# Kernel tuning notes

Hardware: AMD Instinct MI355X
Metric: run time of the kernel (lower is better)

## Reference

```python
import jax, jax.numpy as jnp
import numpy as np

L, D, H, T, B = 4, 512, 8, 1024, 8
FF = 4 * D          # 2048
E = 2
EC = E * D          # 1024 conv channels
K = 31
W = 64              # attention window
DH = D // H
EPS = 1e-5


def _ln(x, g, b):
    m = jnp.mean(x, axis=-1, keepdims=True)
    v = jnp.mean((x - m) ** 2, axis=-1, keepdims=True)
    return (x - m) * jax.lax.rsqrt(v + EPS) * g + b


def setup_inputs() -> dict:
    key = jax.random.key(0)
    ks = iter(jax.random.split(key, 64))
    n = lambda shape, s=0.02: jax.random.normal(next(ks), shape, dtype=jnp.float32) * s
    inp = {
        'x': jax.random.normal(next(ks), (B, T, D), dtype=jnp.float32),
        # FFN1 (half residual)
        'ffn1_ln_g': jnp.ones((L, D)), 'ffn1_ln_b': jnp.zeros((L, D)),
        'ffn1_w1': n((L, D, FF)), 'ffn1_b1': jnp.zeros((L, FF)),
        'ffn1_w2': n((L, FF, D)), 'ffn1_b2': jnp.zeros((L, D)),
        # local MHSA
        'attn_ln_g': jnp.ones((L, D)), 'attn_ln_b': jnp.zeros((L, D)),
        'qkv_w': n((L, D, 3 * D)), 'qkv_b': jnp.zeros((L, 3 * D)),
        'outp_w': n((L, D, D)), 'outp_b': jnp.zeros((L, D)),
        # conv module
        'conv_ln_g': jnp.ones((L, D)), 'conv_ln_b': jnp.zeros((L, D)),
        'pw1_w': n((L, D, 2 * EC)), 'pw1_b': jnp.zeros((L, 2 * EC)),
        'dw_w': n((L, EC, 1, K), 0.1), 'dw_b': jnp.zeros((L, EC)),
        'gn_g': jnp.ones((L, EC)), 'gn_b': jnp.zeros((L, EC)),
        'pw2_w': n((L, EC, D)), 'pw2_b': jnp.zeros((L, D)),
        # FFN2 (half residual)
        'ffn2_ln_g': jnp.ones((L, D)), 'ffn2_ln_b': jnp.zeros((L, D)),
        'ffn2_w1': n((L, D, FF)), 'ffn2_b1': jnp.zeros((L, FF)),
        'ffn2_w2': n((L, FF, D)), 'ffn2_b2': jnp.zeros((L, D)),
        # per-block final LN and decoder final LN
        'blk_ln_g': jnp.ones((L, D)), 'blk_ln_b': jnp.zeros((L, D)),
        'final_ln_g': jnp.ones((D,)), 'final_ln_b': jnp.zeros((D,)),
    }
    return inp


def _forward(x, ffn1_ln_g, ffn1_ln_b, ffn1_w1, ffn1_b1, ffn1_w2, ffn1_b2,
             attn_ln_g, attn_ln_b, qkv_w, qkv_b, outp_w, outp_b,
             conv_ln_g, conv_ln_b, pw1_w, pw1_b, dw_w, dw_b, gn_g, gn_b, pw2_w, pw2_b,
             ffn2_ln_g, ffn2_ln_b, ffn2_w1, ffn2_b1, ffn2_w2, ffn2_b2,
             blk_ln_g, blk_ln_b, final_ln_g, final_ln_b):
    t = jnp.arange(T)
    local_ok = jnp.abs(t[:, None] - t[None, :]) <= (W // 2)   # [T,T] banded window mask
    scale = DH ** -0.5

    for l in range(L):
        # ---- FFN1 (half residual), SiLU ----
        h = _ln(x, ffn1_ln_g[l], ffn1_ln_b[l])
        h = jax.nn.silu(h @ ffn1_w1[l] + ffn1_b1[l]) @ ffn1_w2[l] + ffn1_b2[l]
        x = x + 0.5 * h

        # ---- local windowed MHSA ----
        a = _ln(x, attn_ln_g[l], attn_ln_b[l])
        qkv = (a @ qkv_w[l] + qkv_b[l]).reshape(B, T, 3, H, DH)
        q, k, v = (qkv[:, :, 0].transpose(0, 2, 1, 3),  # [B,H,T,DH]
                   qkv[:, :, 1].transpose(0, 2, 1, 3),
                   qkv[:, :, 2].transpose(0, 2, 1, 3))
        scores = jnp.einsum('bhqd,bhkd->bhqk', q, k) * scale
        scores = jnp.where(local_ok, scores, -jnp.inf)
        attn = jax.nn.softmax(scores, axis=-1)
        o = jnp.einsum('bhqk,bhkd->bhqd', attn, v)
        o = o.transpose(0, 2, 1, 3).reshape(B, T, D)
        x = x + (o @ outp_w[l] + outp_b[l])

        # ---- convolution module ----
        c = _ln(x, conv_ln_g[l], conv_ln_b[l])
        c = c @ pw1_w[l] + pw1_b[l]                 # [B,T,2EC]
        c = c[..., :EC] * jax.nn.sigmoid(c[..., EC:])  # GLU (channel halves)
        c = c.transpose(0, 2, 1)                    # [B,EC,T]
        c = jax.lax.conv_general_dilated(
            c, dw_w[l], window_strides=(1,), padding=[((K - 1) // 2, (K - 1) // 2)],
            dimension_numbers=('NCH', 'OIH', 'NCH'), feature_group_count=EC)
        c = c + dw_b[l][None, :, None]
        # GroupNorm(num_groups=1): normalize over (C,T) per sample
        m = jnp.mean(c, axis=(1, 2), keepdims=True)
        vv = jnp.mean((c - m) ** 2, axis=(1, 2), keepdims=True)
        c = (c - m) * jax.lax.rsqrt(vv + EPS) * gn_g[l][None, :, None] + gn_b[l][None, :, None]
        c = jax.nn.silu(c)
        c = c.transpose(0, 2, 1) @ pw2_w[l] + pw2_b[l]  # [B,T,D]
        x = x + c

        # ---- FFN2 (half residual) ----
        h = _ln(x, ffn2_ln_g[l], ffn2_ln_b[l])
        h = jax.nn.silu(h @ ffn2_w1[l] + ffn2_b1[l]) @ ffn2_w2[l] + ffn2_b2[l]
        x = x + 0.5 * h

        # ---- per-block final LayerNorm ----
        x = _ln(x, blk_ln_g[l], blk_ln_b[l])

    return _ln(x, final_ln_g, final_ln_b)


def reference(x, ffn1_ln_g, ffn1_ln_b, ffn1_w1, ffn1_b1, ffn1_w2, ffn1_b2,
              attn_ln_g, attn_ln_b, qkv_w, qkv_b, outp_w, outp_b,
              conv_ln_g, conv_ln_b, pw1_w, pw1_b, dw_w, dw_b, gn_g, gn_b, pw2_w, pw2_b,
              ffn2_ln_g, ffn2_ln_b, ffn2_w1, ffn2_b1, ffn2_w2, ffn2_b2,
              blk_ln_g, blk_ln_b, final_ln_g, final_ln_b):
    return _forward(x, ffn1_ln_g, ffn1_ln_b, ffn1_w1, ffn1_b1, ffn1_w2, ffn1_b2,
                    attn_ln_g, attn_ln_b, qkv_w, qkv_b, outp_w, outp_b,
                    conv_ln_g, conv_ln_b, pw1_w, pw1_b, dw_w, dw_b, gn_g, gn_b, pw2_w, pw2_b,
                    ffn2_ln_g, ffn2_ln_b, ffn2_w1, ffn2_b1, ffn2_w2, ffn2_b2,
                    blk_ln_g, blk_ln_b, final_ln_g, final_ln_b)
```

## Files before the change

kernel.cpp:

```cpp
#include <hip/hip_runtime.h>
#include <hip/hip_bf16.h>
#include <math.h>

#define L_ 4
#define D_ 512
#define H_ 8
#define T_ 1024
#define B_ 8
#define FF_ 2048
#define EC_ 1024
#define KW_ 31
#define DH_ 64
#define ROWS (B_*T_)

typedef __attribute__((ext_vector_type(8))) short short8;
typedef __attribute__((ext_vector_type(4))) float f32x4;
typedef __attribute__((ext_vector_type(4))) unsigned short ushort4v;
typedef __attribute__((ext_vector_type(2))) unsigned short ushort2v;

static __device__ __forceinline__ unsigned short f2bf(float f) {
  __hip_bfloat16 h = __float2bfloat16(f);
  unsigned short u;
  __builtin_memcpy(&u, &h, 2);
  return u;
}
static __device__ __forceinline__ float bf2f(unsigned short h) {
  union { unsigned u; float f; } v; v.u = ((unsigned)h) << 16;
  return v.f;
}
static __device__ __forceinline__ float sigm(float x) {
  return __builtin_amdgcn_rcpf(1.0f + __expf(-x));
}

#define GLDS(gp, lp) __builtin_amdgcn_global_load_lds( \
    (const __attribute__((address_space(1))) unsigned int*)(const void*)(gp), \
    (__attribute__((address_space(3))) unsigned int*)(void*)(lp), 16, 0, 0)

#define SW8(row, slot) ((slot) ^ (((row) ^ ((row) >> 3)) & 7))

__global__ __launch_bounds__(256) void cvt_kernel(const float* __restrict__ in,
                                                  unsigned short* __restrict__ out)
{
  size_t i = ((size_t)blockIdx.x * 256 + threadIdx.x) * 8;
  float4 v0 = *(const float4*)(in + i);
  float4 v1 = *(const float4*)(in + i + 4);
  float vv[8] = {v0.x, v0.y, v0.z, v0.w, v1.x, v1.y, v1.z, v1.w};
  short8 o;
#pragma unroll
  for (int j = 0; j < 8; ++j) o[j] = (short)f2bf(vv[j]);
  *(short8*)(out + i) = o;
}

__global__ __launch_bounds__(256) void ln_bf16_kernel(const unsigned short* __restrict__ x,
    const float* __restrict__ g, const float* __restrict__ b, unsigned short* __restrict__ y)
{
  int row = blockIdx.x * 4 + (threadIdx.x >> 6);
  int l = threadIdx.x & 63;
  short8 xr = *(const short8*)(x + (size_t)row * D_ + l * 8);
  float vv[8];
#pragma unroll
  for (int j = 0; j < 8; ++j) vv[j] = bf2f((unsigned short)xr[j]);
  float s = 0.f, s2 = 0.f;
#pragma unroll
  for (int j = 0; j < 8; ++j) { s += vv[j]; s2 += vv[j] * vv[j]; }
#pragma unroll
  for (int off = 32; off; off >>= 1) {
    s  += __shfl_xor(s,  off, 64);
    s2 += __shfl_xor(s2, off, 64);
  }
  float mean = s * (1.0f / D_);
  float var  = s2 * (1.0f / D_) - mean * mean;
  float r = __builtin_amdgcn_rsqf(var + 1e-5f);
  float4 g0 = *(const float4*)(g + l * 8);
  float4 g1 = *(const float4*)(g + l * 8 + 4);
  float4 b0 = *(const float4*)(b + l * 8);
  float4 b1 = *(const float4*)(b + l * 8 + 4);
  float gg[8] = {g0.x, g0.y, g0.z, g0.w, g1.x, g1.y, g1.z, g1.w};
  float bb[8] = {b0.x, b0.y, b0.z, b0.w, b1.x, b1.y, b1.z, b1.w};
  short8 o;
#pragma unroll
  for (int j = 0; j < 8; ++j) o[j] = (short)f2bf((vv[j] - mean) * r * gg[j] + bb[j]);
  *(short8*)(y + (size_t)row * D_ + l * 8) = o;
}

template<bool BF2>
__global__ __launch_bounds__(256) void ln_dual_kernel(const unsigned short* __restrict__ x,
    const float* __restrict__ g1, const float* __restrict__ b1,
    const float* __restrict__ g2, const float* __restrict__ b2,
    unsigned short* __restrict__ y1, void* __restrict__ y2)
{
  int row = blockIdx.x * 4 + (threadIdx.x >> 6);
  int l = threadIdx.x & 63;
  short8 xr = *(const short8*)(x + (size_t)row * D_ + l * 8);
  float vv[8];
#pragma unroll
  for (int j = 0; j < 8; ++j) vv[j] = bf2f((unsigned short)xr[j]);
  float s = 0.f, s2 = 0.f;
#pragma unroll
  for (int j = 0; j < 8; ++j) { s += vv[j]; s2 += vv[j] * vv[j]; }
#pragma unroll
  for (int off = 32; off; off >>= 1) {
    s  += __shfl_xor(s,  off, 64);
    s2 += __shfl_xor(s2, off, 64);
  }
  float mean = s * (1.0f / D_);
  float var  = s2 * (1.0f / D_) - mean * mean;
  float r = __builtin_amdgcn_rsqf(var + 1e-5f);
  float4 g0 = *(const float4*)(g1 + l * 8);
  float4 g1v = *(const float4*)(g1 + l * 8 + 4);
  float4 b0 = *(const float4*)(b1 + l * 8);
  float4 b1v = *(const float4*)(b1 + l * 8 + 4);
  float ga[8] = {g0.x, g0.y, g0.z, g0.w, g1v.x, g1v.y, g1v.z, g1v.w};
  float ba[8] = {b0.x, b0.y, b0.z, b0.w, b1v.x, b1v.y, b1v.z, b1v.w};
  float yv[8];
  float u = 0.f, u2 = 0.f;
#pragma unroll
  for (int j = 0; j < 8; ++j) {
    yv[j] = (vv[j] - mean) * r * ga[j] + ba[j];
    u += yv[j]; u2 += yv[j] * yv[j];
  }
  {
    short8 o;
#pragma unroll
    for (int j = 0; j < 8; ++j) o[j] = (short)f2bf(yv[j]);
    *(short8*)(y1 + (size_t)row * D_ + l * 8) = o;
  }
#pragma unroll
  for (int off = 32; off; off >>= 1) {
    u  += __shfl_xor(u,  off, 64);
    u2 += __shfl_xor(u2, off, 64);
  }
  float mean2 = u * (1.0f / D_);
  float var2  = u2 * (1.0f / D_) - mean2 * mean2;
  float r2 = __builtin_amdgcn_rsqf(var2 + 1e-5f);
  float4 c0 = *(const float4*)(g2 + l * 8);
  float4 c1 = *(const float4*)(g2 + l * 8 + 4);
  float4 d0 = *(const float4*)(b2 + l * 8);
  float4 d1 = *(const float4*)(b2 + l * 8 + 4);
  float gc[8] = {c0.x, c0.y, c0.z, c0.w, c1.x, c1.y, c1.z, c1.w};
  float bc[8] = {d0.x, d0.y, d0.z, d0.w, d1.x, d1.y, d1.z, d1.w};
  if constexpr (BF2) {
    short8 o;
#pragma unroll
    for (int j = 0; j < 8; ++j) o[j] = (short)f2bf((yv[j] - mean2) * r2 * gc[j] + bc[j]);
    *(short8*)((unsigned short*)y2 + (size_t)row * D_ + l * 8) = o;
  } else {
    float z[8];
#pragma unroll
    for (int j = 0; j < 8; ++j) z[j] = (yv[j] - mean2) * r2 * gc[j] + bc[j];
    float4 o0 = {z[0], z[1], z[2], z[3]};
    float4 o1 = {z[4], z[5], z[6], z[7]};
    float* yp = (float*)y2 + (size_t)row * D_ + l * 8;
    *(float4*)yp = o0; *(float4*)(yp + 4) = o1;
  }
}

__global__ __launch_bounds__(256) void wtr_kernel(const float* __restrict__ W,
    unsigned short* __restrict__ Wt, int K, int N)
{
  __shared__ float tile[32][33];
  const float* Wl = W + (size_t)blockIdx.z * K * N;
  unsigned short* Wtl = Wt + (size_t)blockIdx.z * K * N;
  int n0 = blockIdx.x * 32, k0 = blockIdx.y * 32;
  int c = threadIdx.x & 31, r = threadIdx.x >> 5;
#pragma unroll
  for (int it = 0; it < 4; ++it) {
    int kk = r + it * 8;
    tile[kk][c] = Wl[(size_t)(k0 + kk) * N + n0 + c];
  }
  __syncthreads();
#pragma unroll
  for (int it = 0; it < 4; ++it) {
    int nn = r + it * 8;
    Wtl[(size_t)(n0 + nn) * K + k0 + c] = f2bf(tile[c][nn]);
  }
}

template<int EPI>
__global__ __launch_bounds__(256) void gemm_mfma(
    const unsigned short* __restrict__ A, const unsigned short* __restrict__ Wt,
    const float* __restrict__ bias, void* __restrict__ Cv,
    int N, int K)
{
  constexpr int TM = 128;
  constexpr int AI = TM / 32;
  __shared__ __align__(16) unsigned short As[3][TM * 32];
  __shared__ __align__(16) unsigned short Bs[3][128 * 32];
  int t = threadIdx.x;
  int gx = gridDim.x;
  int nwg = gx * gridDim.y;
  int orig = blockIdx.y * gx + blockIdx.x;
  int lg = (orig & 7) * (nwg >> 3) + (orig >> 3);
  int row0 = (lg / gx) * TM;
  int col0 = (lg % gx) * (EPI == 3 ? 64 : 128);
  int l = t & 63, w = t >> 6, wm = w >> 1, wn = w & 1;

  int ar0 = t >> 2;
  int sa0 = (t & 3) ^ ((ar0 >> 1) & 3);
  int ar1 = (t + 256) >> 2;
  int sa1 = (t & 3) ^ ((ar1 >> 1) & 3);
  const unsigned short* agp0 = A + (size_t)(row0 + ar0) * K + sa0 * 8;
  const unsigned short* agp1 = A + (size_t)(row0 + ar1) * K + sa1 * 8;
  const unsigned short* bgp0 = Wt + (size_t)(col0 + ar0) * K + sa0 * 8;
  const unsigned short* bgp1 =
      (EPI == 3) ? Wt + (size_t)(EC_ + col0 + (ar1 - 64)) * K + sa1 * 8
                 : Wt + (size_t)(col0 + ar1) * K + sa1 * 8;

  int lrow = (l >> 4) * 4, lcol = l & 15, kq = l >> 4;
  int aoff[AI], boff[4];
#pragma unroll
  for (int i = 0; i < AI; ++i) {
    int row = wm * (TM / 2) + i * 16 + lcol;
    aoff[i] = (row * 4 + (kq ^ ((row >> 1) & 3))) * 8;
  }
#pragma unroll
  for (int j = 0; j < 4; ++j) {
    int row;
    if constexpr (EPI == 3)
      row = (j < 2 ? wn * 32 + j * 16 : 64 + wn * 32 + (j - 2) * 16) + lcol;
    else
      row = wn * 64 + j * 16 + lcol;
    boff[j] = (row * 4 + (kq ^ ((row >> 1) & 3))) * 8;
  }

  f32x4 acc[AI][4] = {};
  int nt = K >> 5;

  auto stage = [&](int buf) {
    GLDS(agp0, As[buf] + t * 8);
    GLDS(agp1, As[buf] + (t + 256) * 8);
    GLDS(bgp0, Bs[buf] + t * 8);
    GLDS(bgp1, Bs[buf] + (t + 256) * 8);
    agp0 += 32; agp1 += 32; bgp0 += 32; bgp1 += 32;
  };
  stage(0); stage(1);
  int cur = 0, nxt = 2;

  for (int kt = 0; kt < nt; ++kt) {
    if (kt < nt - 1) asm volatile("s_waitcnt vmcnt(4)" ::: "memory");
    else             asm volatile("s_waitcnt vmcnt(0)" ::: "memory");
    __builtin_amdgcn_s_barrier();
    __builtin_amdgcn_sched_barrier(0);
    if (kt + 2 < nt) { stage(nxt); nxt = (nxt == 2) ? 0 : nxt + 1; }
    const unsigned short* Ab = As[cur];
    const unsigned short* Bb = Bs[cur];
    cur = (cur == 2) ? 0 : cur + 1;
    short8 af[AI], bfr[4];
#pragma unroll
    for (int i = 0; i < AI; ++i) af[i]  = *(const short8*)(Ab + aoff[i]);
#pragma unroll
    for (int j = 0; j < 4; ++j) bfr[j] = *(const short8*)(Bb + boff[j]);
    __builtin_amdgcn_s_setprio(1);
#pragma unroll
    for (int i = 0; i < AI; ++i)
#pragma unroll
      for (int j = 0; j < 4; ++j)
        acc[i][j] = __builtin_amdgcn_mfma_f32_16x16x32_bf16(af[i], bfr[j], acc[i][j], 0, 0, 0);
    __builtin_amdgcn_s_setprio(0);
  }

  if constexpr (EPI == 3) {
    float bja[2], bjg[2];
#pragma unroll
    for (int j = 0; j < 2; ++j) {
      int c = col0 + wn * 32 + j * 16 + lcol;
      bja[j] = bias[c];
      bjg[j] = bias[EC_ + c];
    }
#pragma unroll
    for (int i = 0; i < AI; ++i) {
      int gr0 = row0 + wm * (TM / 2) + i * 16 + lrow;
#pragma unroll
      for (int j = 0; j < 2; ++j) {
        int gc = col0 + wn * 32 + j * 16 + lcol;
#pragma unroll
        for (int q = 0; q < 4; ++q) {
          float a = acc[i][j][q] + bja[j];
          float g = acc[i][j + 2][q] + bjg[j];
          ((unsigned short*)Cv)[(size_t)(gr0 + q) * N + gc] = f2bf(a * sigm(g));
        }
      }
    }
  } else {
    float bj[4];
#pragma unroll
    for (int j = 0; j < 4; ++j) bj[j] = bias[col0 + wn * 64 + j * 16 + lcol];
#pragma unroll
    for (int i = 0; i < AI; ++i) {
      int gr0 = row0 + wm * (TM / 2) + i * 16 + lrow;
#pragma unroll
      for (int j = 0; j < 4; ++j) {
        int gc = col0 + wn * 64 + j * 16 + lcol;
#pragma unroll
        for (int q = 0; q < 4; ++q) {
          float v = acc[i][j][q] + bj[j];
          size_t off = (size_t)(gr0 + q) * N + gc;
          if constexpr (EPI == 0) {
            ((unsigned short*)Cv)[off] = f2bf(v);
          } else {
            ((unsigned short*)Cv)[off] = f2bf(v * sigm(v));
          }
        }
      }
    }
  }
}

__global__ __launch_bounds__(256) void gemm_res64(
    const unsigned short* __restrict__ A, const unsigned short* __restrict__ Wt,
    const float* __restrict__ bias, const unsigned short* __restrict__ R,
    unsigned short* __restrict__ C, int N, int K, float alpha)
{
  __shared__ __align__(16) unsigned short As[3][64 * 64];
  __shared__ __align__(16) unsigned short Bs[3][128 * 64];
  int t = threadIdx.x;
  int gx = gridDim.x;
  int nwg = gx * gridDim.y;
  int orig = blockIdx.y * gx + blockIdx.x;
  int lg = (orig & 7) * (nwg >> 3) + (orig >> 3);
  int row0 = (lg / gx) * 64;
  int col0 = (lg % gx) * 128;
  int l = t & 63, w = t >> 6, wm = w >> 1, wn = w & 1;

  int arA0 = t >> 3;
  int sA0  = (t & 7) ^ (arA0 & 7);
  int cA1  = t + 256;
  int arA1 = cA1 >> 3;
  int sA1  = (cA1 & 7) ^ (arA1 & 7);
  const unsigned short* agp0 = A + (size_t)(row0 + arA0) * K + sA0 * 8;
  const unsigned short* agp1 = A + (size_t)(row0 + arA1) * K + sA1 * 8;
  const unsigned short* bgp[4];
#pragma unroll
  for (int q = 0; q < 4; ++q) {
    int c = t + q * 256;
    int r = c >> 3, s = (c & 7) ^ (r & 7);
    bgp[q] = Wt + (size_t)(col0 + r) * K + s * 8;
  }

  int lcol = l & 15, kq = l >> 4, lrow = kq * 4;
  int aoff[2][2], boff[4][2];
#pragma unroll
  for (int i = 0; i < 2; ++i) {
    int row = wm * 32 + i * 16 + lcol;
#pragma unroll
    for (int kk = 0; kk < 2; ++kk)
      aoff[i][kk] = row * 64 + (((kk * 4 + kq) ^ (row & 7)) * 8);
  }
#pragma unroll
  for (int j = 0; j < 4; ++j) {
    int row = wn * 64 + j * 16 + lcol;
#pragma unroll
    for (int kk = 0; kk < 2; ++kk)
      boff[j][kk] = row * 64 + (((kk * 4 + kq) ^ (row & 7)) * 8);
  }

  f32x4 acc[2][4] = {};
  int nt = K >> 6;

  auto stage = [&](int buf) {
    GLDS(agp0, As[buf] + t * 8);
    GLDS(agp1, As[buf] + (t + 256) * 8);
#pragma unroll
    for (int q = 0; q < 4; ++q) GLDS(bgp[q], Bs[buf] + (t + q * 256) * 8);
    agp0 += 64; agp1 += 64;
#pragma unroll
    for (int q = 0; q < 4; ++q) bgp[q] += 64;
  };
  stage(0); stage(1);
  int cur = 0, nxt = 2;

  for (int kt = 0; kt < nt; ++kt) {
    if (kt < nt - 1) asm volatile("s_waitcnt vmcnt(6)" ::: "memory");
    else             asm volatile("s_waitcnt vmcnt(0)" ::: "memory");
    __builtin_amdgcn_s_barrier();
    __builtin_amdgcn_sched_barrier(0);
    if (kt + 2 < nt) { stage(nxt); nxt = (nxt == 2) ? 0 : nxt + 1; }
    const unsigned short* Ab = As[cur];
    const unsigned short* Bb = Bs[cur];
    cur = (cur == 2) ? 0 : cur + 1;
    short8 af[2][2], bfr[4][2];
#pragma unroll
    for (int i = 0; i < 2; ++i)
#pragma unroll
      for (int kk = 0; kk < 2; ++kk) af[i][kk] = *(const short8*)(Ab + aoff[i][kk]);
#pragma unroll
    for (int j = 0; j < 4; ++j)
#pragma unroll
      for (int kk = 0; kk < 2; ++kk) bfr[j][kk] = *(const short8*)(Bb + boff[j][kk]);
    __builtin_amdgcn_s_setprio(1);
#pragma unroll
    for (int kk = 0; kk < 2; ++kk)
#pragma unroll
      for (int i = 0; i < 2; ++i)
#pragma unroll
        for (int j = 0; j < 4; ++j)
          acc[i][j] = __builtin_amdgcn_mfma_f32_16x16x32_bf16(af[i][kk], bfr[j][kk],
                                                              acc[i][j], 0, 0, 0);
    __builtin_amdgcn_s_setprio(0);
  }

  float bj[4];
#pragma unroll
  for (int j = 0; j < 4; ++j) bj[j] = bias[col0 + wn * 64 + j * 16 + lcol];
#pragma unroll
  for (int i = 0; i < 2; ++i) {
    int gr0 = row0 + wm * 32 + i * 16 + lrow;
#pragma unroll
    for (int j = 0; j < 4; ++j) {
      int gc = col0 + wn * 64 + j * 16 + lcol;
#pragma unroll
      for (int q = 0; q < 4; ++q) {
        size_t off = (size_t)(gr0 + q) * N + gc;
        C[off] = f2bf(bf2f(R[off]) + alpha * (acc[i][j][q] + bj[j]));
      }
    }
  }
}

__global__ __launch_bounds__(256) void attn_kernel(const unsigned short* __restrict__ QKV,
                                                   unsigned short* __restrict__ O)
{
  __shared__ __align__(16) unsigned short Ks[128 * 64];
  __shared__ __align__(16) unsigned short Vt[64 * 128];
  __shared__ __align__(16) unsigned short Ps[64 * 128];
  int qt = blockIdx.x, h = blockIdx.y, b = blockIdx.z;
  int t = threadIdx.x;
  int l = t & 63, w = t >> 6;
  int q0 = qt * 64;
  int jbase = q0 - 32;

#pragma unroll
  for (int i = 0; i < 4; ++i) {
    int c = t + i * 256;
    int row = c >> 3, sl = c & 7;
    int jg = jbase + row;
    short8 kv = {};
    if ((unsigned)jg < (unsigned)T_)
      kv = *(const short8*)(QKV + ((size_t)(b * T_ + jg)) * 1536 + 512 + h * DH_ + sl * 8);
    *(short8*)(Ks + row * 64 + SW8(row, sl) * 8) = kv;
  }
#pragma unroll
  for (int i = 0; i < 4; ++i) {
    int c = t + i * 256;
    int row = c >> 3, d0 = (c & 7) * 8;
    int jg = jbase + row;
    short8 vv = {};
    if ((unsigned)jg < (unsigned)T_)
      vv = *(const short8*)(QKV + ((size_t)(b * T_ + jg)) * 1536 + 1024 + h * DH_ + d0);
#pragma unroll
    for (int q = 0; q < 8; ++q) {
      int d = d0 + q;
      Vt[d * 128 + SW8(d, row >> 3) * 8 + (row & 7)] = (unsigned short)vv[q];
    }
  }
  short8 qf[2];
#pragma unroll
  for (int ks = 0; ks < 2; ++ks)
    qf[ks] = *(const short8*)(QKV + ((size_t)(b * T_ + q0 + w * 16 + (l & 15))) * 1536
                              + h * DH_ + ks * 32 + (l >> 4) * 8);
  __syncthreads();

  f32x4 sacc[8] = {};
#pragma unroll
  for (int jt = 0; jt < 8; ++jt) {
#pragma unroll
    for (int ks = 0; ks < 2; ++ks) {
      int row = jt * 16 + (l & 15);
      int sl = ks * 4 + (l >> 4);
      short8 kf = *(const short8*)(Ks + row * 64 + SW8(row, sl) * 8);
      sacc[jt] = __builtin_amdgcn_mfma_f32_16x16x32_bf16(qf[ks], kf, sacc[jt], 0, 0, 0);
    }
  }

  const float scale = 0.125f;
  int qgl0 = q0 + w * 16 + ((l >> 4) << 2);
  int jl = jbase + (l & 15);
  float m4[4] = {-3.0e38f, -3.0e38f, -3.0e38f, -3.0e38f};
#pragma unroll
  for (int jt = 0; jt < 8; ++jt) {
#pragma unroll
    for (int r = 0; r < 4; ++r) {
      float s = sacc[jt][r] * scale;
      int jg = jl + jt * 16;
      int dd = jg - (qgl0 + r);
      bool ok = ((unsigned)jg < (unsigned)T_) && (dd <= 32) && (dd >= -32);
      s = ok ? s : -3.0e38f;
      sacc[jt][r] = s;
      m4[r] = fmaxf(m4[r], s);
    }
  }
#pragma unroll
  for (int r = 0; r < 4; ++r) {
    m4[r] = fmaxf(m4[r], __shfl_xor(m4[r], 1, 64));
    m4[r] = fmaxf(m4[r], __shfl_xor(m4[r], 2, 64));
    m4[r] = fmaxf(m4[r], __shfl_xor(m4[r], 4, 64));
    m4[r] = fmaxf(m4[r], __shfl_xor(m4[r], 8, 64));
  }
  float sum4[4] = {0.f, 0.f, 0.f, 0.f};
#pragma unroll
  for (int jt = 0; jt < 8; ++jt) {
#pragma unroll
    for (int r = 0; r < 4; ++r) {
      float e = __expf(sacc[jt][r] - m4[r]);
      sum4[r] += e;
      int qrow = w * 16 + ((l >> 4) << 2) + r;
      int j = jt * 16 + (l & 15);
      Ps[qrow * 128 + SW8(qrow, j >> 3) * 8 + (j & 7)] = f2bf(e);
    }
  }
#pragma unroll
  for (int r = 0; r < 4; ++r) {
    sum4[r] += __shfl_xor(sum4[r], 1, 64);
    sum4[r] += __shfl_xor(sum4[r], 2, 64);
    sum4[r] += __shfl_xor(sum4[r], 4, 64);
    sum4[r] += __shfl_xor(sum4[r], 8, 64);
    sum4[r] = __builtin_amdgcn_rcpf(sum4[r]);
  }

  f32x4 oacc[4] = {};
#pragma unroll
  for (int ks = 0; ks < 4; ++ks) {
    int prow = w * 16 + (l & 15);
    int sl = ks * 4 + (l >> 4);
    short8 pf = *(const short8*)(Ps + prow * 128 + SW8(prow, sl) * 8);
#pragma unroll
    for (int dt = 0; dt < 4; ++dt) {
      int vrow = dt * 16 + (l & 15);
      short8 vf = *(const short8*)(Vt + vrow * 128 + SW8(vrow, sl) * 8);
      oacc[dt] = __builtin_amdgcn_mfma_f32_16x16x32_bf16(pf, vf, oacc[dt], 0, 0, 0);
    }
  }
#pragma unroll
  for (int dt = 0; dt < 4; ++dt) {
#pragma unroll
    for (int r = 0; r < 4; ++r) {
      int qg = q0 + w * 16 + ((l >> 4) << 2) + r;
      int d = dt * 16 + (l & 15);
      O[((size_t)(b * T_ + qg)) * D_ + h * DH_ + d] = f2bf(oacc[dt][r] * sum4[r]);
    }
  }
}

#define TT_ 16
__global__ __launch_bounds__(256) void dwconv_kernel(const unsigned short* __restrict__ X,
    const float* __restrict__ w, const float* __restrict__ bias,
    unsigned short* __restrict__ Y, float* __restrict__ red)
{
  int t = threadIdx.x;
  int gid = blockIdx.x;
  int ecb = gid & 1;
  int tt  = (gid >> 1) & 63;
  int b   = gid >> 7;
  int e0 = ecb * 512 + t * 2;
  int t0 = tt * TT_;
  const unsigned short* xp = X + (size_t)b * T_ * EC_ + e0;

  float wr0[KW_], wr1[KW_];
#pragma unroll
  for (int k = 0; k < KW_; ++k) { wr0[k] = w[e0 * KW_ + k]; wr1[k] = w[(e0 + 1) * KW_ + k]; }
  float out0[TT_], out1[TT_];
  float bv0 = bias[e0], bv1 = bias[e0 + 1];
#pragma unroll
  for (int i = 0; i < TT_; ++i) { out0[i] = bv0; out1[i] = bv1; }

#pragma unroll
  for (int j = 0; j < TT_ + KW_ - 1; ++j) {
    int tj = t0 - 15 + j;
    float x0 = 0.f, x1 = 0.f;
    if ((unsigned)tj < (unsigned)T_) {
      ushort2v u = *(const ushort2v*)(xp + (size_t)tj * EC_);
      x0 = bf2f(u.x); x1 = bf2f(u.y);
    }
#pragma unroll
    for (int i = 0; i < TT_; ++i) {
      int k = j - i;
      if (k >= 0 && k < KW_) {
        out0[i] = fmaf(x0, wr0[k], out0[i]);
        out1[i] = fmaf(x1, wr1[k], out1[i]);
      }
    }
  }
  unsigned short* yp = Y + ((size_t)b * T_ + t0) * EC_ + e0;
  float s = 0.f, s2 = 0.f;
#pragma unroll
  for (int i = 0; i < TT_; ++i) {
    ushort2v o; o.x = f2bf(out0[i]); o.y = f2bf(out1[i]);
    *(ushort2v*)(yp + (size_t)i * EC_) = o;
    s += out0[i] + out1[i];
    s2 += out0[i] * out0[i] + out1[i] * out1[i];
  }
#pragma unroll
  for (int off = 32; off; off >>= 1) {
    s  += __shfl_down(s,  off, 64);
    s2 += __shfl_down(s2, off, 64);
  }
  __shared__ float rs[4], rq[4];
  if ((t & 63) == 0) { rs[t >> 6] = s; rq[t >> 6] = s2; }
  __syncthreads();
  if (t == 0) {
    int loc = gid & 127;
    red[(b * 128 + loc) * 2]     = rs[0] + rs[1] + rs[2] + rs[3];
    red[(b * 128 + loc) * 2 + 1] = rq[0] + rq[1] + rq[2] + rq[3];
  }
}

__global__ __launch_bounds__(256) void gn_stats_kernel(const float* __restrict__ partial,
                                                       float* __restrict__ stats)
{
  int b = blockIdx.x, t = threadIdx.x;
  float s = 0.f, s2 = 0.f;
  if (t < 128) {
    s  = partial[b * 256 + t * 2];
    s2 = partial[b * 256 + t * 2 + 1];
  }
#pragma unroll
  for (int off = 32; off; off >>= 1) {
    s  += __shfl_down(s,  off, 64);
    s2 += __shfl_down(s2, off, 64);
  }
  __shared__ float rs[4], rq[4];
  if ((t & 63) == 0) { rs[t >> 6] = s; rq[t >> 6] = s2; }
  __syncthreads();
  if (t == 0) {
    float S = rs[0] + rs[1] + rs[2] + rs[3];
    float S2 = rq[0] + rq[1] + rq[2] + rq[3];
    const float n = (float)(T_ * EC_);
    float mean = S / n;
    float var  = S2 / n - mean * mean;
    stats[b * 2]     = mean;
    stats[b * 2 + 1] = __builtin_amdgcn_rsqf(var + 1e-5f);
  }
}

__global__ __launch_bounds__(256) void gn_apply_kernel(const unsigned short* __restrict__ X,
    const float* __restrict__ stats, const float* __restrict__ g, const float* __restrict__ bb,
    unsigned short* __restrict__ out)
{
  int idx = blockIdx.x * 256 + threadIdx.x;
  int e4 = (idx & 255) << 2;
  int bt = idx >> 8;
  int b  = bt >> 10;
  float mean = stats[b * 2], rstd = stats[b * 2 + 1];
  ushort4v v = *(const ushort4v*)(X + (size_t)idx * 4);
  float4 gv = *(const float4*)(g + e4);
  float4 bv = *(const float4*)(bb + e4);
  float gg[4] = {gv.x, gv.y, gv.z, gv.w};
  float bbv[4] = {bv.x, bv.y, bv.z, bv.w};
  ushort4v o;
#pragma unroll
  for (int j = 0; j < 4; ++j) {
    float u = (bf2f(v[j]) - mean) * rstd * gg[j] + bbv[j];
    o[j] = f2bf(u * sigm(u));
  }
  *(ushort4v*)(out + (size_t)idx * 4) = o;
}

extern "C" void kernel_launch(void* const* d_in, const int* in_sizes, int n_in,
                              void* d_out, int out_size, void* d_ws, size_t ws_size,
                              hipStream_t stream)
{
  const float* in_x      = (const float*)d_in[0];
  const float* ffn1_ln_g = (const float*)d_in[1];
  const float* ffn1_ln_b = (const float*)d_in[2];
  const float* ffn1_w1   = (const float*)d_in[3];
  const float* ffn1_b1   = (const float*)d_in[4];
  const float* ffn1_w2   = (const float*)d_in[5];
  const float* ffn1_b2   = (const float*)d_in[6];
  const float* attn_ln_g = (const float*)d_in[7];
  const float* attn_ln_b = (const float*)d_in[8];
  const float* qkv_w     = (const float*)d_in[9];
  const float* qkv_b     = (const float*)d_in[10];
  const float* outp_w    = (const float*)d_in[11];
  const float* outp_b    = (const float*)d_in[12];
  const float* conv_ln_g = (const float*)d_in[13];
  const float* conv_ln_b = (const float*)d_in[14];
  const float* pw1_w     = (const float*)d_in[15];
  const float* pw1_b     = (const float*)d_in[16];
  const float* dw_w      = (const float*)d_in[17];
  const float* dw_b      = (const float*)d_in[18];
  const float* gn_g      = (const float*)d_in[19];
  const float* gn_b      = (const float*)d_in[20];
  const float* pw2_w     = (const float*)d_in[21];
  const float* pw2_b     = (const float*)d_in[22];
  const float* ffn2_ln_g = (const float*)d_in[23];
  const float* ffn2_ln_b = (const float*)d_in[24];
  const float* ffn2_w1   = (const float*)d_in[25];
  const float* ffn2_b1   = (const float*)d_in[26];
  const float* ffn2_w2   = (const float*)d_in[27];
  const float* ffn2_b2   = (const float*)d_in[28];
  const float* blk_ln_g  = (const float*)d_in[29];
  const float* blk_ln_b  = (const float*)d_in[30];
  const float* fin_ln_g  = (const float*)d_in[31];
  const float* fin_ln_b  = (const float*)d_in[32];

  char* p = (char*)d_ws;
  unsigned short* x    = (unsigned short*)p; p += (size_t)ROWS * D_ * 2;
  unsigned short* big3 = (unsigned short*)p; p += (size_t)ROWS * EC_ * 2;
  float* red  = (float*)p;          p += 8192 * 4;
  unsigned short* abuf  = (unsigned short*)p; p += (size_t)ROWS * D_ * 2;
  unsigned short* inner = (unsigned short*)p; p += (size_t)ROWS * FF_ * 2;
  unsigned short* big2  = (unsigned short*)p; p += (size_t)ROWS * EC_ * 2;
  unsigned short* wt_w1a = (unsigned short*)p; p += (size_t)L_ * D_ * FF_ * 2;
  unsigned short* wt_w1b = (unsigned short*)p; p += (size_t)L_ * FF_ * D_ * 2;
  unsigned short* wt_qkv = (unsigned short*)p; p += (size_t)L_ * D_ * 1536 * 2;
  unsigned short* wt_out = (unsigned short*)p; p += (size_t)L_ * D_ * D_ * 2;
  unsigned short* wt_pw1 = (unsigned short*)p; p += (size_t)L_ * D_ * 2048 * 2;
  unsigned short* wt_pw2 = (unsigned short*)p; p += (size_t)L_ * EC_ * D_ * 2;
  unsigned short* wt_w2a = (unsigned short*)p; p += (size_t)L_ * D_ * FF_ * 2;
  unsigned short* wt_w2b = (unsigned short*)p; p += (size_t)L_ * FF_ * D_ * 2;
  float* stats = red + 4096;

  dim3 blk256(256);
  cvt_kernel<<<ROWS * D_ / (256 * 8), blk256, 0, stream>>>(in_x, x);

  wtr_kernel<<<dim3(FF_/32,  D_/32,  L_), blk256, 0, stream>>>(ffn1_w1, wt_w1a, D_, FF_);
  wtr_kernel<<<dim3(D_/32,   FF_/32, L_), blk256, 0, stream>>>(ffn1_w2, wt_w1b, FF_, D_);
  wtr_kernel<<<dim3(1536/32, D_/32,  L_), blk256, 0, stream>>>(qkv_w,   wt_qkv, D_, 1536);
  wtr_kernel<<<dim3(D_/32,   D_/32,  L_), blk256, 0, stream>>>(outp_w,  wt_out, D_, D_);
  wtr_kernel<<<dim3(2048/32, D_/32,  L_), blk256, 0, stream>>>(pw1_w,   wt_pw1, D_, 2048);
  wtr_kernel<<<dim3(D_/32,   EC_/32, L_), blk256, 0, stream>>>(pw2_w,   wt_pw2, EC_, D_);
  wtr_kernel<<<dim3(FF_/32,  D_/32,  L_), blk256, 0, stream>>>(ffn2_w1, wt_w2a, D_, FF_);
  wtr_kernel<<<dim3(D_/32,   FF_/32, L_), blk256, 0, stream>>>(ffn2_w2, wt_w2b, FF_, D_);

  ln_bf16_kernel<<<ROWS/4, blk256, 0, stream>>>(x, ffn1_ln_g, ffn1_ln_b, abuf);

  for (int l = 0; l < L_; ++l) {
    gemm_mfma<1><<<dim3(FF_/128, ROWS/128), blk256, 0, stream>>>(
        abuf, wt_w1a + (size_t)l*D_*FF_, ffn1_b1 + l*FF_, inner, FF_, D_);
    gemm_res64<<<dim3(D_/128, ROWS/64), blk256, 0, stream>>>(
        inner, wt_w1b + (size_t)l*FF_*D_, ffn1_b2 + l*D_, x, x, D_, FF_, 0.5f);

    ln_bf16_kernel<<<ROWS/4, blk256, 0, stream>>>(x, attn_ln_g + l*D_, attn_ln_b + l*D_, abuf);
    gemm_mfma<0><<<dim3(1536/128, ROWS/128), blk256, 0, stream>>>(
        abuf, wt_qkv + (size_t)l*D_*1536, qkv_b + l*1536, inner, 1536, D_);
    attn_kernel<<<dim3(T_/64, H_, B_), blk256, 0, stream>>>(inner, abuf);
    gemm_res64<<<dim3(D_/128, ROWS/64), blk256, 0, stream>>>(
        abuf, wt_out + (size_t)l*D_*D_, outp_b + l*D_, x, x, D_, D_, 1.0f);

    ln_bf16_kernel<<<ROWS/4, blk256, 0, stream>>>(x, conv_ln_g + l*D_, conv_ln_b + l*D_, abuf);
    gemm_mfma<3><<<dim3(EC_/64, ROWS/128), blk256, 0, stream>>>(
        abuf, wt_pw1 + (size_t)l*D_*2048, pw1_b + l*2048, big2, EC_, D_);
    dwconv_kernel<<<B_ * (T_/TT_) * (EC_/512), blk256, 0, stream>>>(
        big2, dw_w + (size_t)l*EC_*KW_, dw_b + l*EC_, big3, red);
    gn_stats_kernel<<<B_, blk256, 0, stream>>>(red, stats);
    gn_apply_kernel<<<(ROWS * EC_ / 4) / 256, blk256, 0, stream>>>(
        big3, stats, gn_g + l*EC_, gn_b + l*EC_, big2);
    gemm_res64<<<dim3(D_/128, ROWS/64), blk256, 0, stream>>>(
        big2, wt_pw2 + (size_t)l*EC_*D_, pw2_b + l*D_, x, x, D_, EC_, 1.0f);

    ln_bf16_kernel<<<ROWS/4, blk256, 0, stream>>>(x, ffn2_ln_g + l*D_, ffn2_ln_b + l*D_, abuf);
    gemm_mfma<1><<<dim3(FF_/128, ROWS/128), blk256, 0, stream>>>(
        abuf, wt_w2a + (size_t)l*D_*FF_, ffn2_b1 + l*FF_, inner, FF_, D_);
    gemm_res64<<<dim3(D_/128, ROWS/64), blk256, 0, stream>>>(
        inner, wt_w2b + (size_t)l*FF_*D_, ffn2_b2 + l*D_, x, x, D_, FF_, 0.5f);

    if (l < L_ - 1) {
      ln_dual_kernel<true><<<ROWS/4, blk256, 0, stream>>>(
          x, blk_ln_g + l*D_, blk_ln_b + l*D_,
          ffn1_ln_g + (l+1)*D_, ffn1_ln_b + (l+1)*D_, x, abuf);
    } else {
      ln_dual_kernel<false><<<ROWS/4, blk256, 0, stream>>>(
          x, blk_ln_g + l*D_, blk_ln_b + l*D_, fin_ln_g, fin_ln_b, x, d_out);
    }
  }
}
```

Measured before the change: 1.155 ms.

## Fuse input conversion with first LN, vectorize GN apply, prioritize attention MFMA

Merges the initial fp32-to-bf16 conversion with the first LayerNorm into one kernel, so one launch and one full read of the residual stream go away. The GroupNorm apply kernel now handles 8 elements per thread with 16-byte loads and stores, and launches half as many blocks. The attention kernel raises wave priority with s_setprio around its two MFMA loops. These are small, unrelated tweaks, so each gain is likely minor.

```diff
diff --git a/kernel.cpp b/kernel.cpp
--- a/kernel.cpp
+++ b/kernel.cpp
@@ -38,17 +38,46 @@
 
 #define SW8(row, slot) ((slot) ^ (((row) ^ ((row) >> 3)) & 7))
 
-__global__ __launch_bounds__(256) void cvt_kernel(const float* __restrict__ in,
-                                                  unsigned short* __restrict__ out)
-{
-  size_t i = ((size_t)blockIdx.x * 256 + threadIdx.x) * 8;
-  float4 v0 = *(const float4*)(in + i);
-  float4 v1 = *(const float4*)(in + i + 4);
-  float vv[8] = {v0.x, v0.y, v0.z, v0.w, v1.x, v1.y, v1.z, v1.w};
+__global__ __launch_bounds__(256) void cvt_ln_kernel(const float* __restrict__ in,
+    const float* __restrict__ g, const float* __restrict__ b,
+    unsigned short* __restrict__ x, unsigned short* __restrict__ y)
+{
+  int row = blockIdx.x * 4 + (threadIdx.x >> 6);
+  int l = threadIdx.x & 63;
+  const float* ir = in + (size_t)row * D_ + l * 8;
+  float4 v0 = *(const float4*)ir;
+  float4 v1 = *(const float4*)(ir + 4);
+  float raw[8] = {v0.x, v0.y, v0.z, v0.w, v1.x, v1.y, v1.z, v1.w};
+  short8 xo;
+  float vv[8];
+#pragma unroll
+  for (int j = 0; j < 8; ++j) {
+    unsigned short h = f2bf(raw[j]);
+    xo[j] = (short)h;
+    vv[j] = bf2f(h);
+  }
+  *(short8*)(x + (size_t)row * D_ + l * 8) = xo;
+  float s = 0.f, s2 = 0.f;
+#pragma unroll
+  for (int j = 0; j < 8; ++j) { s += vv[j]; s2 += vv[j] * vv[j]; }
+#pragma unroll
+  for (int off = 32; off; off >>= 1) {
+    s  += __shfl_xor(s,  off, 64);
+    s2 += __shfl_xor(s2, off, 64);
+  }
+  float mean = s * (1.0f / D_);
+  float var  = s2 * (1.0f / D_) - mean * mean;
+  float r = __builtin_amdgcn_rsqf(var + 1e-5f);
+  float4 g0 = *(const float4*)(g + l * 8);
+  float4 g1 = *(const float4*)(g + l * 8 + 4);
+  float4 b0 = *(const float4*)(b + l * 8);
+  float4 b1 = *(const float4*)(b + l * 8 + 4);
+  float gg[8] = {g0.x, g0.y, g0.z, g0.w, g1.x, g1.y, g1.z, g1.w};
+  float bb[8] = {b0.x, b0.y, b0.z, b0.w, b1.x, b1.y, b1.z, b1.w};
   short8 o;
 #pragma unroll
-  for (int j = 0; j < 8; ++j) o[j] = (short)f2bf(vv[j]);
-  *(short8*)(out + i) = o;
+  for (int j = 0; j < 8; ++j) o[j] = (short)f2bf((vv[j] - mean) * r * gg[j] + bb[j]);
+  *(short8*)(y + (size_t)row * D_ + l * 8) = o;
 }
 
 __global__ __launch_bounds__(256) void ln_bf16_kernel(const unsigned short* __restrict__ x,
@@ -461,6 +490,7 @@
   __syncthreads();
 
   f32x4 sacc[8] = {};
+  __builtin_amdgcn_s_setprio(1);
 #pragma unroll
   for (int jt = 0; jt < 8; ++jt) {
 #pragma unroll
@@ -471,6 +501,7 @@
       sacc[jt] = __builtin_amdgcn_mfma_f32_16x16x32_bf16(qf[ks], kf, sacc[jt], 0, 0, 0);
     }
   }
+  __builtin_amdgcn_s_setprio(0);
 
   const float scale = 0.125f;
   int qgl0 = q0 + w * 16 + ((l >> 4) << 2);
@@ -518,6 +549,7 @@
   }
 
   f32x4 oacc[4] = {};
+  __builtin_amdgcn_s_setprio(1);
 #pragma unroll
   for (int ks = 0; ks < 4; ++ks) {
     int prow = w * 16 + (l & 15);
@@ -530,6 +562,7 @@
       oacc[dt] = __builtin_amdgcn_mfma_f32_16x16x32_bf16(pf, vf, oacc[dt], 0, 0, 0);
     }
   }
+  __builtin_amdgcn_s_setprio(0);
 #pragma unroll
   for (int dt = 0; dt < 4; ++dt) {
 #pragma unroll
@@ -637,22 +670,24 @@
     unsigned short* __restrict__ out)
 {
   int idx = blockIdx.x * 256 + threadIdx.x;
-  int e4 = (idx & 255) << 2;
-  int bt = idx >> 8;
+  int e8 = (idx & 127) << 3;
+  int bt = idx >> 7;
   int b  = bt >> 10;
   float mean = stats[b * 2], rstd = stats[b * 2 + 1];
-  ushort4v v = *(const ushort4v*)(X + (size_t)idx * 4);
-  float4 gv = *(const float4*)(g + e4);
-  float4 bv = *(const float4*)(bb + e4);
-  float gg[4] = {gv.x, gv.y, gv.z, gv.w};
-  float bbv[4] = {bv.x, bv.y, bv.z, bv.w};
-  ushort4v o;
-#pragma unroll
-  for (int j = 0; j < 4; ++j) {
-    float u = (bf2f(v[j]) - mean) * rstd * gg[j] + bbv[j];
-    o[j] = f2bf(u * sigm(u));
-  }
-  *(ushort4v*)(out + (size_t)idx * 4) = o;
+  short8 v = *(const short8*)(X + (size_t)idx * 8);
+  float4 g0 = *(const float4*)(g + e8);
+  float4 g1 = *(const float4*)(g + e8 + 4);
+  float4 b0 = *(const float4*)(bb + e8);
+  float4 b1 = *(const float4*)(bb + e8 + 4);
+  float gg[8] = {g0.x, g0.y, g0.z, g0.w, g1.x, g1.y, g1.z, g1.w};
+  float bv[8] = {b0.x, b0.y, b0.z, b0.w, b1.x, b1.y, b1.z, b1.w};
+  short8 o;
+#pragma unroll
+  for (int j = 0; j < 8; ++j) {
+    float u = (bf2f((unsigned short)v[j]) - mean) * rstd * gg[j] + bv[j];
+    o[j] = (short)f2bf(u * sigm(u));
+  }
+  *(short8*)(out + (size_t)idx * 8) = o;
 }
 
 extern "C" void kernel_launch(void* const* d_in, const int* in_sizes, int n_in,
@@ -711,7 +746,7 @@
   float* stats = red + 4096;
 
   dim3 blk256(256);
-  cvt_kernel<<<ROWS * D_ / (256 * 8), blk256, 0, stream>>>(in_x, x);
+  cvt_ln_kernel<<<ROWS/4, blk256, 0, stream>>>(in_x, ffn1_ln_g, ffn1_ln_b, x, abuf);
 
   wtr_kernel<<<dim3(FF_/32,  D_/32,  L_), blk256, 0, stream>>>(ffn1_w1, wt_w1a, D_, FF_);
   wtr_kernel<<<dim3(D_/32,   FF_/32, L_), blk256, 0, stream>>>(ffn1_w2, wt_w1b, FF_, D_);
@@ -722,8 +757,6 @@
   wtr_kernel<<<dim3(FF_/32,  D_/32,  L_), blk256, 0, stream>>>(ffn2_w1, wt_w2a, D_, FF_);
   wtr_kernel<<<dim3(D_/32,   FF_/32, L_), blk256, 0, stream>>>(ffn2_w2, wt_w2b, FF_, D_);
 
-  ln_bf16_kernel<<<ROWS/4, blk256, 0, stream>>>(x, ffn1_ln_g, ffn1_ln_b, abuf);
-
   for (int l = 0; l < L_; ++l) {
     gemm_mfma<1><<<dim3(FF_/128, ROWS/128), blk256, 0, stream>>>(
         abuf, wt_w1a + (size_t)l*D_*FF_, ffn1_b1 + l*FF_, inner, FF_, D_);
@@ -743,7 +776,7 @@
     dwconv_kernel<<<B_ * (T_/TT_) * (EC_/512), blk256, 0, stream>>>(
         big2, dw_w + (size_t)l*EC_*KW_, dw_b + l*EC_, big3, red);
     gn_stats_kernel<<<B_, blk256, 0, stream>>>(red, stats);
-    gn_apply_kernel<<<(ROWS * EC_ / 4) / 256, blk256, 0, stream>>>(
+    gn_apply_kernel<<<(ROWS * EC_ / 8) / 256, blk256, 0, stream>>>(
         big3, stats, gn_g + l*EC_, gn_b + l*EC_, big2);
     gemm_res64<<<dim3(D_/128, ROWS/64), blk256, 0, stream>>>(
         big2, wt_pw2 + (size_t)l*EC_*D_, pw2_b + l*D_, x, x, D_, EC_, 1.0f);
```

Measured after the change: 1.156 ms. About the same (+0.1%).
